# Kernel optimization log

Hardware: AMD Instinct MI355X
Metric: run time of the kernel (lower is better)

The kernel has to match this reference:

```python
import jax, jax.numpy as jnp
import numpy as np
import math

D = 1024      # d_model
H = 4096      # expert hidden
E = 8         # num_experts
K = 2         # top_k
CAP_FACTOR = 1.25
B, S = 4, 2048
T = B * S
CAP = int(math.ceil(CAP_FACTOR * T * K / E))  # 2560


def setup_inputs() -> dict:
    key = jax.random.key(0)
    ks = jax.random.split(key, 6)
    x  = jax.random.normal(ks[0], (B, S, D), dtype=jnp.float32)
    Wr = jax.random.normal(ks[1], (D, E), dtype=jnp.float32) * (1.0 / np.sqrt(D))
    W1 = jax.random.normal(ks[2], (E, D, H), dtype=jnp.float32) * (1.0 / np.sqrt(D))
    b1 = jnp.zeros((E, H), dtype=jnp.float32)
    W2 = jax.random.normal(ks[3], (E, H, D), dtype=jnp.float32) * (1.0 / np.sqrt(H))
    b2 = jnp.zeros((E, D), dtype=jnp.float32)
    return {"x": x, "Wr": Wr, "W1": W1, "b1": b1, "W2": W2, "b2": b2}


def reference(x, Wr, W1, b1, W2, b2):
    x_flat = x.reshape(T, D)

    # ---- Router: top-k softmax gating (temp = 1.0), renormalized weights ----
    logits = jnp.einsum('td,de->te', x_flat, Wr)
    probs = jax.nn.softmax(logits, axis=-1)
    topk_w, topk_idx = jax.lax.top_k(probs, K)            # [T,K]
    topk_w = topk_w / jnp.sum(topk_w, axis=-1, keepdims=True)

    # ---- Vectorized capacity-based dispatch ----
    e = topk_idx.reshape(-1)                               # [T*K] expert id per pair
    onehot = jax.nn.one_hot(e, E, dtype=jnp.int32)         # [T*K, E]
    pos_all = jnp.cumsum(onehot, axis=0) - 1               # slot within expert
    pos = jnp.take_along_axis(pos_all, e[:, None], axis=1)[:, 0]
    keep = pos < CAP
    # dropped pairs go to a dummy slot E*CAP (sliced off / zero-padded)
    dest = jnp.where(keep, e * CAP + pos, E * CAP)         # [T*K]

    x_pairs = jnp.repeat(x_flat, K, axis=0)                # [T*K, D]
    buf = jnp.zeros((E * CAP + 1, D), dtype=x.dtype).at[dest].set(x_pairs)
    expert_in = buf[:E * CAP].reshape(E, CAP, D)

    # ---- Grouped expert MLP (GELU) ----
    h = jax.nn.gelu(jnp.einsum('ecd,edh->ech', expert_in, W1) + b1[:, None, :])
    expert_out = jnp.einsum('ech,ehd->ecd', h, W2) + b2[:, None, :]

    # ---- Combine: gather back and weight; dropped tokens get zeros ----
    out_pad = jnp.concatenate(
        [expert_out.reshape(E * CAP, D), jnp.zeros((1, D), dtype=x.dtype)], axis=0)
    y_pairs = out_pad[dest] * topk_w.reshape(-1)[:, None]  # [T*K, D]
    y_flat = y_pairs.reshape(T, K, D).sum(axis=1)
    return y_flat.reshape(B, S, D)
```

## Files before the change

kernel.cpp:

```cpp
#include <hip/hip_runtime.h>
#include <stdint.h>

#define D_MODEL 1024
#define H_DIM   4096
#define NE      8
#define NCAP    2560
#define NTOK    8192
#define NPAIR   (NTOK * 2)

typedef __attribute__((ext_vector_type(8))) __bf16 bf16x8;
typedef __attribute__((ext_vector_type(4))) float  f32x4;
typedef __attribute__((ext_vector_type(8))) unsigned short ushort8;

__device__ __forceinline__ unsigned short f2bf(float f) {
  union { float f; unsigned u; } v; v.f = f;
  unsigned r = v.u + 0x7fffu + ((v.u >> 16) & 1u);
  return (unsigned short)(r >> 16);
}
__device__ __forceinline__ float bf2f(unsigned short s) {
  union { unsigned u; float f; } v; v.u = ((unsigned)s) << 16;
  return v.f;
}
__device__ __forceinline__ float gelu_tanh(float x) {
  float u = 0.7978845608028654f * (x + 0.044715f * x * x * x);
  float e = __expf(2.0f * u);
  float th = 1.0f - 2.0f / (e + 1.0f);
  return 0.5f * x * (1.0f + th);
}
__device__ __forceinline__ void load_lds16(const void* g, void* l) {
  __builtin_amdgcn_global_load_lds(
      (const __attribute__((address_space(1))) unsigned int*)g,
      (__attribute__((address_space(3))) unsigned int*)l, 16, 0, 0);
}

__global__ __launch_bounds__(256) void router_kernel(
    const float* __restrict__ x, const float* __restrict__ Wr,
    int* __restrict__ pair_e, float* __restrict__ pair_w) {
  int lane = threadIdx.x & 63;
  int t = blockIdx.x * 4 + (threadIdx.x >> 6);
  float acc[NE];
#pragma unroll
  for (int e = 0; e < NE; ++e) acc[e] = 0.0f;
  const float* xr = x + (size_t)t * D_MODEL;
  for (int d = lane; d < D_MODEL; d += 64) {
    float xv = xr[d];
#pragma unroll
    for (int e = 0; e < NE; ++e) acc[e] = fmaf(xv, Wr[d * NE + e], acc[e]);
  }
#pragma unroll
  for (int off = 32; off > 0; off >>= 1) {
#pragma unroll
    for (int e = 0; e < NE; ++e) acc[e] += __shfl_down(acc[e], off, 64);
  }
  if (lane == 0) {
    int i1 = 0;
#pragma unroll
    for (int e = 1; e < NE; ++e) if (acc[e] > acc[i1]) i1 = e;
    int i2 = (i1 == 0) ? 1 : 0;
#pragma unroll
    for (int e = 0; e < NE; ++e) if (e != i1 && acc[e] > acc[i2]) i2 = e;
    float p2 = expf(acc[i2] - acc[i1]);
    float inv = 1.0f / (1.0f + p2);
    pair_e[t * 2]     = i1;  pair_e[t * 2 + 1] = i2;
    pair_w[t * 2]     = inv;
    pair_w[t * 2 + 1] = p2 * inv;
  }
}

__global__ __launch_bounds__(1024) void assign_kernel(
    const int* __restrict__ pair_e, int* __restrict__ pair_dest,
    int* __restrict__ counts) {
  __shared__ int wtot[16][NE];
  const int tid = threadIdx.x;
  const int lane = tid & 63, w = tid >> 6;

  int ids[16];
  const int4* pe = (const int4*)(pair_e + tid * 16);
#pragma unroll
  for (int q = 0; q < 4; ++q) {
    int4 v = pe[q];
    ids[q * 4 + 0] = v.x; ids[q * 4 + 1] = v.y;
    ids[q * 4 + 2] = v.z; ids[q * 4 + 3] = v.w;
  }
  int c[NE];
#pragma unroll
  for (int e = 0; e < NE; ++e) c[e] = 0;
#pragma unroll
  for (int j = 0; j < 16; ++j) c[ids[j]]++;

  int incl[NE];
#pragma unroll
  for (int e = 0; e < NE; ++e) incl[e] = c[e];
#pragma unroll
  for (int d = 1; d < 64; d <<= 1) {
#pragma unroll
    for (int e = 0; e < NE; ++e) {
      int u = __shfl_up(incl[e], d, 64);
      if (lane >= d) incl[e] += u;
    }
  }
  if (lane == 63) {
#pragma unroll
    for (int e = 0; e < NE; ++e) wtot[w][e] = incl[e];
  }
  __syncthreads();
  if (tid < NE) {
    int run = 0;
#pragma unroll
    for (int ww = 0; ww < 16; ++ww) {
      int t2 = wtot[ww][tid];
      wtot[ww][tid] = run;
      run += t2;
    }
    counts[tid] = run < NCAP ? run : NCAP;
  }
  __syncthreads();

  int off[NE];
#pragma unroll
  for (int e = 0; e < NE; ++e) off[e] = wtot[w][e] + incl[e] - c[e];
#pragma unroll
  for (int j = 0; j < 16; ++j) {
    int e = ids[j];
    int pos = off[e]++;
    pair_dest[tid * 16 + j] = (pos < NCAP) ? (e * NCAP + pos) : (NE * NCAP);
  }
}

__global__ __launch_bounds__(64) void dispatch_kernel(
    const float* __restrict__ x, const int* __restrict__ pair_dest,
    unsigned short* __restrict__ Xd) {
  int i = blockIdx.x;
  int dest = pair_dest[i];
  if (dest >= NE * NCAP) return;
  int lane = threadIdx.x;
  int t = i >> 1;
  const float4* xr = (const float4*)(x + (size_t)t * D_MODEL);
  ushort4* dr = (ushort4*)(Xd + (size_t)dest * D_MODEL);
#pragma unroll
  for (int c = 0; c < 4; ++c) {
    float4 v = xr[lane + c * 64];
    ushort4 o;
    o.x = f2bf(v.x); o.y = f2bf(v.y); o.z = f2bf(v.z); o.w = f2bf(v.w);
    dr[lane + c * 64] = o;
  }
}

__global__ __launch_bounds__(256) void transpose_cvt(
    const float* __restrict__ src, unsigned short* __restrict__ dst,
    int R, int C) {
  __shared__ float tile[64][65];
  int e = blockIdx.z;
  int c0 = blockIdx.x * 64, r0 = blockIdx.y * 64;
  int col = threadIdx.x & 63, rr = threadIdx.x >> 6;
  const float* s = src + (size_t)e * R * C;
#pragma unroll
  for (int it = 0; it < 16; ++it) {
    int row = it * 4 + rr;
    tile[row][col] = s[(size_t)(r0 + row) * C + c0 + col];
  }
  __syncthreads();
  unsigned short* d = dst + (size_t)e * R * C;
#pragma unroll
  for (int it = 0; it < 16; ++it) {
    int crow = it * 4 + rr;
    d[(size_t)(c0 + crow) * R + r0 + col] = f2bf(tile[col][crow]);
  }
}

__global__ __launch_bounds__(256, 4) void moe_gemm(
    const unsigned short* __restrict__ Abase,
    const unsigned short* __restrict__ Bbase,
    const float* __restrict__ bias,
    unsigned short* __restrict__ Cout,
    const int* __restrict__ counts,
    int M, int N, int K, int NBM, int do_gelu) {
  __shared__ char smem[32768];
  const int e = blockIdx.z;
  int r = blockIdx.x;
  int grp = r >> 4, lid = r & 15;
  int mg = NBM >> 2;
  int gm = grp % mg, gn = grp / mg;
  const int m0 = (gm * 4 + (lid & 3)) * 128;
  const int n0 = (gn * 4 + (lid >> 2)) * 128;
  const int cnt = counts[e];
  if (m0 >= cnt) return;

  const int tid = threadIdx.x;
  const int lane = tid & 63;
  const int wid = tid >> 6;
  const int wm = (wid & 1) * 64;
  const int wn = (wid >> 1) * 64;

  const unsigned short* A = Abase + (size_t)e * M * K;
  const unsigned short* B = Bbase + (size_t)e * N * K;

  f32x4 acc[4][4];
  f32x4 zero = {0.f, 0.f, 0.f, 0.f};
#pragma unroll
  for (int i = 0; i < 4; ++i)
#pragma unroll
    for (int j = 0; j < 4; ++j) acc[i][j] = zero;

  char* As = smem;
  char* Bs = smem + 16384;

  const unsigned short* ga[4];
  const unsigned short* gb[4];
  int ldso[4];
#pragma unroll
  for (int c = 0; c < 4; ++c) {
    int ci = c * 256 + wid * 64 + lane;
    int srow = ci >> 3;
    int sgc = (ci & 7) ^ (srow & 7);
    ga[c] = A + (size_t)(m0 + srow) * K + sgc * 8;
    gb[c] = B + (size_t)(n0 + srow) * K + sgc * 8;
    ldso[c] = (c * 256 + wid * 64) * 16;
  }

  const int KT = K >> 6;
  for (int kt = 0; kt < KT; ++kt) {
#pragma unroll
    for (int c = 0; c < 4; ++c) {
      load_lds16(ga[c], As + ldso[c]);
      ga[c] += 64;
      load_lds16(gb[c], Bs + ldso[c]);
      gb[c] += 64;
    }
    __syncthreads();
#pragma unroll
    for (int kk = 0; kk < 2; ++kk) {
      bf16x8 af[4], bfr[4];
      int lc = kk * 4 + (lane >> 4);
#pragma unroll
      for (int f = 0; f < 4; ++f) {
        int ar = wm + f * 16 + (lane & 15);
        af[f] = *(const bf16x8*)(As + ar * 128 + ((lc ^ (ar & 7)) * 16));
        int br = wn + f * 16 + (lane & 15);
        bfr[f] = *(const bf16x8*)(Bs + br * 128 + ((lc ^ (br & 7)) * 16));
      }
#pragma unroll
      for (int i = 0; i < 4; ++i)
#pragma unroll
        for (int j = 0; j < 4; ++j)
          acc[i][j] = __builtin_amdgcn_mfma_f32_16x16x32_bf16(
              af[i], bfr[j], acc[i][j], 0, 0, 0);
    }
    __syncthreads();
  }

  const float* be = bias + (size_t)e * N;
#pragma unroll
  for (int i = 0; i < 4; ++i) {
    int rbase = wm + i * 16 + (lane >> 4) * 4;
#pragma unroll
    for (int j = 0; j < 4; ++j) {
      int col = wn + j * 16 + (lane & 15);
      float bv = be[n0 + col];
#pragma unroll
      for (int r2 = 0; r2 < 4; ++r2) {
        float xv = acc[i][j][r2] + bv;
        if (do_gelu) xv = gelu_tanh(xv);
        *(unsigned short*)(smem + (rbase + r2) * 256 + col * 2) = f2bf(xv);
      }
    }
  }
  __syncthreads();
  const int r16 = tid >> 4, c16 = tid & 15;
#pragma unroll
  for (int it = 0; it < 8; ++it) {
    int row = it * 16 + r16;
    ushort8 v = *(const ushort8*)(smem + row * 256 + c16 * 16);
    *(ushort8*)(Cout + ((size_t)e * M + m0 + row) * N + n0 + c16 * 8) = v;
  }
}

__global__ __launch_bounds__(256) void combine_kernel(
    const unsigned short* __restrict__ Ebuf,
    const int* __restrict__ pair_dest,
    const float* __restrict__ pair_w,
    float* __restrict__ out) {
  int t = blockIdx.x;
  int d0 = threadIdx.x * 4;
  float4 r = {0.f, 0.f, 0.f, 0.f};
#pragma unroll
  for (int k = 0; k < 2; ++k) {
    int dest = pair_dest[t * 2 + k];
    if (dest < NE * NCAP) {
      float w = pair_w[t * 2 + k];
      ushort4 v = *(const ushort4*)(Ebuf + (size_t)dest * D_MODEL + d0);
      r.x += w * bf2f(v.x); r.y += w * bf2f(v.y);
      r.z += w * bf2f(v.z); r.w += w * bf2f(v.w);
    }
  }
  *(float4*)(out + (size_t)t * D_MODEL + d0) = r;
}

extern "C" void kernel_launch(void* const* d_in, const int* in_sizes, int n_in,
                              void* d_out, int out_size, void* d_ws, size_t ws_size,
                              hipStream_t stream) {
  const float* x  = (const float*)d_in[0];
  const float* Wr = (const float*)d_in[1];
  const float* W1 = (const float*)d_in[2];
  const float* b1 = (const float*)d_in[3];
  const float* W2 = (const float*)d_in[4];
  const float* b2 = (const float*)d_in[5];
  float* out = (float*)d_out;

  char* ws = (char*)d_ws;
  unsigned short* W1T  = (unsigned short*)(ws + 0);
  unsigned short* W2T  = (unsigned short*)(ws + 67108864);
  unsigned short* Xd   = (unsigned short*)(ws + 134217728);
  unsigned short* Ebuf = Xd;
  unsigned short* Hbuf = (unsigned short*)(ws + 176160768);
  int*   pair_e    = (int*)(ws + 343932928);
  float* pair_w    = (float*)(ws + 343998464);
  int*   pair_dest = (int*)(ws + 344064000);
  int*   counts    = (int*)(ws + 344129536);

  transpose_cvt<<<dim3(H_DIM / 64, D_MODEL / 64, NE), 256, 0, stream>>>(W1, W1T, D_MODEL, H_DIM);
  transpose_cvt<<<dim3(D_MODEL / 64, H_DIM / 64, NE), 256, 0, stream>>>(W2, W2T, H_DIM, D_MODEL);

  router_kernel<<<NTOK / 4, 256, 0, stream>>>(x, Wr, pair_e, pair_w);
  assign_kernel<<<1, 1024, 0, stream>>>(pair_e, pair_dest, counts);
  dispatch_kernel<<<NPAIR, 64, 0, stream>>>(x, pair_dest, Xd);

  moe_gemm<<<dim3((NCAP / 128) * (H_DIM / 128), 1, NE), 256, 0, stream>>>(
      Xd, W1T, b1, Hbuf, counts, NCAP, H_DIM, D_MODEL, NCAP / 128, 1);
  moe_gemm<<<dim3((NCAP / 128) * (D_MODEL / 128), 1, NE), 256, 0, stream>>>(
      Hbuf, W2T, b2, Ebuf, counts, NCAP, D_MODEL, H_DIM, NCAP / 128, 0);

  combine_kernel<<<NTOK, 256, 0, stream>>>(Ebuf, pair_dest, pair_w, out);
}
```

Baseline: 768.6 us.

## Add 256x256-tile first-layer MoE GEMM and vectorize weight transpose

Adds a dedicated first-layer expert GEMM kernel with 256x256 output tiles, 512 threads, 128KB double-buffered LDS with XOR swizzle, and an LDS-staged coalesced epilogue that applies bias and GELU. Larger tiles raise arithmetic intensity and cut global traffic per FLOP, at the cost of lower occupancy and coarser early exit on partially filled experts. The weight transpose/convert kernel is also rewritten to use float4 loads and 16-byte bf16 stores with a padded tile to reduce memory transactions.

```diff
diff --git a/kernel.cpp b/kernel.cpp
--- a/kernel.cpp
+++ b/kernel.cpp
@@ -149,22 +149,168 @@
 __global__ __launch_bounds__(256) void transpose_cvt(
     const float* __restrict__ src, unsigned short* __restrict__ dst,
     int R, int C) {
-  __shared__ float tile[64][65];
+  __shared__ float tile[64][69];
   int e = blockIdx.z;
   int c0 = blockIdx.x * 64, r0 = blockIdx.y * 64;
-  int col = threadIdx.x & 63, rr = threadIdx.x >> 6;
-  const float* s = src + (size_t)e * R * C;
+  const float* s = src + (size_t)e * R * C + (size_t)r0 * C + c0;
+  int tc = (threadIdx.x & 15) * 4;
+  int tr = threadIdx.x >> 4;
+#pragma unroll
+  for (int it = 0; it < 4; ++it) {
+    int row = tr + it * 16;
+    float4 v = *(const float4*)(s + (size_t)row * C + tc);
+    tile[row][tc]     = v.x; tile[row][tc + 1] = v.y;
+    tile[row][tc + 2] = v.z; tile[row][tc + 3] = v.w;
+  }
+  __syncthreads();
+  unsigned short* d = dst + (size_t)e * R * C + (size_t)c0 * R + r0;
+  int oc  = threadIdx.x >> 3;
+  int orr = (threadIdx.x & 7) * 8;
+#pragma unroll
+  for (int it = 0; it < 2; ++it) {
+    int crow = oc + it * 32;
+    ushort8 v;
+#pragma unroll
+    for (int j = 0; j < 8; ++j) v[j] = f2bf(tile[orr + j][crow]);
+    *(ushort8*)(d + (size_t)crow * R + orr) = v;
+  }
+}
+
+__global__ __launch_bounds__(512, 2) void moe_gemm1(
+    const unsigned short* __restrict__ Abase,
+    const unsigned short* __restrict__ Bbase,
+    const float* __restrict__ bias,
+    unsigned short* __restrict__ Cout,
+    const int* __restrict__ counts) {
+  const int M = NCAP, N = H_DIM, K = D_MODEL;
+  const int KT = K >> 6;
+  __shared__ char smem[131072];
+  const int e = blockIdx.z;
+  int r = blockIdx.x;
+  int grp = r >> 2, lid = r & 3;
+  int gm = grp % 5, gn = grp / 5;
+  const int m0 = (gm * 2 + (lid & 1)) * 256;
+  const int n0 = (gn * 2 + (lid >> 1)) * 256;
+  if (m0 >= counts[e]) return;
+
+  const int tid = threadIdx.x;
+  const int lane = tid & 63;
+  const int wid = tid >> 6;
+  const int wm = (wid >> 2) * 128;
+  const int wn = (wid & 3) * 64;
+
+  const unsigned short* A = Abase + (size_t)e * M * K;
+  const unsigned short* B = Bbase + (size_t)e * N * K;
+
+  f32x4 acc[8][4];
+  f32x4 zero = {0.f, 0.f, 0.f, 0.f};
+#pragma unroll
+  for (int i = 0; i < 8; ++i)
+#pragma unroll
+    for (int j = 0; j < 4; ++j) acc[i][j] = zero;
+
+  const unsigned short* ga[4];
+  const unsigned short* gb[4];
+  int ldso[4];
+#pragma unroll
+  for (int c = 0; c < 4; ++c) {
+    int ci = c * 512 + tid;
+    int row = ci >> 3;
+    int sc = (ci & 7) ^ (row & 7);
+    ga[c] = A + (size_t)(m0 + row) * K + sc * 8;
+    gb[c] = B + (size_t)(n0 + row) * K + sc * 8;
+    ldso[c] = (c * 512 + wid * 64) * 16;
+  }
+
+#pragma unroll
+  for (int c = 0; c < 4; ++c) {
+    load_lds16(ga[c], smem + ldso[c]);          ga[c] += 64;
+    load_lds16(gb[c], smem + 32768 + ldso[c]);  gb[c] += 64;
+  }
+
+  for (int kt = 0; kt < KT; ++kt) {
+    __syncthreads();
+    const char* Ab = smem + (kt & 1) * 65536;
+    const char* Bb = Ab + 32768;
+    if (kt + 1 < KT) {
+      char* An = smem + ((kt + 1) & 1) * 65536;
+#pragma unroll
+      for (int c = 0; c < 4; ++c) {
+        load_lds16(ga[c], An + ldso[c]);          ga[c] += 64;
+        load_lds16(gb[c], An + 32768 + ldso[c]);  gb[c] += 64;
+      }
+    }
+    {
+      bf16x8 af[8], bfr[4];
+      int lc = (lane >> 4);
+#pragma unroll
+      for (int f = 0; f < 8; ++f) {
+        int ar = wm + f * 16 + (lane & 15);
+        af[f] = *(const bf16x8*)(Ab + ar * 128 + ((lc ^ (ar & 7)) * 16));
+      }
+#pragma unroll
+      for (int f = 0; f < 4; ++f) {
+        int br = wn + f * 16 + (lane & 15);
+        bfr[f] = *(const bf16x8*)(Bb + br * 128 + ((lc ^ (br & 7)) * 16));
+      }
+      __builtin_amdgcn_s_setprio(1);
+#pragma unroll
+      for (int i = 0; i < 8; ++i)
+#pragma unroll
+        for (int j = 0; j < 4; ++j)
+          acc[i][j] = __builtin_amdgcn_mfma_f32_16x16x32_bf16(
+              af[i], bfr[j], acc[i][j], 0, 0, 0);
+      __builtin_amdgcn_s_setprio(0);
+    }
+    __builtin_amdgcn_s_barrier();
+    {
+      bf16x8 af[8], bfr[4];
+      int lc = 4 + (lane >> 4);
+#pragma unroll
+      for (int f = 0; f < 8; ++f) {
+        int ar = wm + f * 16 + (lane & 15);
+        af[f] = *(const bf16x8*)(Ab + ar * 128 + ((lc ^ (ar & 7)) * 16));
+      }
+#pragma unroll
+      for (int f = 0; f < 4; ++f) {
+        int br = wn + f * 16 + (lane & 15);
+        bfr[f] = *(const bf16x8*)(Bb + br * 128 + ((lc ^ (br & 7)) * 16));
+      }
+      __builtin_amdgcn_s_setprio(1);
+#pragma unroll
+      for (int i = 0; i < 8; ++i)
+#pragma unroll
+        for (int j = 0; j < 4; ++j)
+          acc[i][j] = __builtin_amdgcn_mfma_f32_16x16x32_bf16(
+              af[i], bfr[j], acc[i][j], 0, 0, 0);
+      __builtin_amdgcn_s_setprio(0);
+    }
+  }
+
+  __syncthreads();
+  const float* be = bias + (size_t)e * N;
+#pragma unroll
+  for (int i = 0; i < 8; ++i) {
+    int rbase = wm + i * 16 + ((lane >> 4) << 2);
+#pragma unroll
+    for (int j = 0; j < 4; ++j) {
+      int col = wn + j * 16 + (lane & 15);
+      float bv = be[n0 + col];
+#pragma unroll
+      for (int r2 = 0; r2 < 4; ++r2) {
+        float xv = acc[i][j][r2] + bv;
+        xv = gelu_tanh(xv);
+        *(unsigned short*)(smem + (size_t)(rbase + r2) * 512 + col * 2) = f2bf(xv);
+      }
+    }
+  }
+  __syncthreads();
 #pragma unroll
   for (int it = 0; it < 16; ++it) {
-    int row = it * 4 + rr;
-    tile[row][col] = s[(size_t)(r0 + row) * C + c0 + col];
-  }
-  __syncthreads();
-  unsigned short* d = dst + (size_t)e * R * C;
-#pragma unroll
-  for (int it = 0; it < 16; ++it) {
-    int crow = it * 4 + rr;
-    d[(size_t)(c0 + crow) * R + r0 + col] = f2bf(tile[col][crow]);
+    int idx = it * 4096 + tid * 8;
+    int row = idx >> 8, col = idx & 255;
+    ushort8 v = *(const ushort8*)(smem + (size_t)idx * 2);
+    *(ushort8*)(Cout + ((size_t)e * M + m0 + row) * N + n0 + col) = v;
   }
 }
 
@@ -325,8 +471,8 @@
   assign_kernel<<<1, 1024, 0, stream>>>(pair_e, pair_dest, counts);
   dispatch_kernel<<<NPAIR, 64, 0, stream>>>(x, pair_dest, Xd);
 
-  moe_gemm<<<dim3((NCAP / 128) * (H_DIM / 128), 1, NE), 256, 0, stream>>>(
-      Xd, W1T, b1, Hbuf, counts, NCAP, H_DIM, D_MODEL, NCAP / 128, 1);
+  moe_gemm1<<<dim3((NCAP / 256) * (H_DIM / 256), 1, NE), 512, 0, stream>>>(
+      Xd, W1T, b1, Hbuf, counts);
   moe_gemm<<<dim3((NCAP / 128) * (D_MODEL / 128), 1, NE), 256, 0, stream>>>(
       Hbuf, W2T, b2, Ebuf, counts, NCAP, D_MODEL, H_DIM, NCAP / 128, 0);
 
```

Result: slower. 807.0 us (+5.0%).
